# Kernel optimization log

Hardware: AMD Instinct MI355X
Metric: run time of the kernel (lower is better)

Reference implementation:

```python
import jax, jax.numpy as jnp
import numpy as np

N = 500000      # total nodes
C = 256         # in_channels
H = 8           # num_heads
D = 32          # out_channels per head
G = 4096        # number of graphs in the batch


def setup_inputs() -> dict:
    key = jax.random.key(0)
    k1, k2, k3, k4, k5 = jax.random.split(key, 5)
    x = jax.random.normal(k1, (N, C), dtype=jnp.float32)
    batch = jnp.sort(jax.random.randint(k2, (N,), 0, G)).astype(jnp.int64)
    Wg = jax.random.normal(k3, (H, C), dtype=jnp.float32) / np.sqrt(C)
    Wn = jax.random.normal(k4, (H, C, D), dtype=jnp.float32) / np.sqrt(C)
    bn = jax.random.normal(k5, (H, D), dtype=jnp.float32) * 0.01
    return {"x": x, "batch": batch, "Wg": Wg, "Wn": Wn, "bn": bn}


def reference(x, batch, Wg, Wn, bn):
    batch = batch.astype(jnp.int32)
    # Gate logits for all heads at once: [N, H]
    gate = x @ Wg.T
    # Segment-wise (per-graph) stable softmax over nodes, per head
    m = jax.ops.segment_max(gate, batch, num_segments=G)        # [G, H]
    e = jnp.exp(gate - m[batch])                                # [N, H]
    s = jax.ops.segment_sum(e, batch, num_segments=G)           # [G, H]
    alpha = e / s[batch]                                        # [N, H]
    # Per-head value projection: [N, H, D]
    v = jnp.einsum('nc,hcd->nhd', x, Wn) + bn
    # Attention-weighted segment sum -> [G, H, D], concat heads -> [G, H*D]
    out = jax.ops.segment_sum(alpha[:, :, None] * v, batch, num_segments=G)
    return out.reshape(G, H * D)
```

## Files before the change

kernel.cpp:

```cpp
#include <hip/hip_runtime.h>
#include <hip/hip_bf16.h>
#include <cmath>

#define NN 500000
#define CC 256
#define HH 8
#define DD 32
#define GG 4096
#define CH 32

#define OFF_START 0
#define OFF_FLAG  16400

__device__ __forceinline__ int get_batch(const void* b, int i, int is64) {
    return is64 ? (int)((const long long*)b)[i] : ((const int*)b)[i];
}

__global__ void detect_kernel(const int* __restrict__ b32, int n, int* __restrict__ flag) {
    if (threadIdx.x == 0 && blockIdx.x == 0) {
        int a = b32[(n / 2) | 1];
        int b = b32[(n - 2) | 1];
        int c = b32[((n / 2) + (n / 4)) | 1];
        *flag = (a == 0 && b == 0 && c == 0) ? 1 : 0;
    }
}

__global__ void seg_offsets_kernel(const void* __restrict__ batch, const int* __restrict__ flag,
                                   int n, int g_total, int* __restrict__ start) {
    int is64 = *flag;
    int i = blockIdx.x * blockDim.x + threadIdx.x;
    if (i >= n) return;
    int b = get_batch(batch, i, is64);
    int prev = (i == 0) ? -1 : get_batch(batch, i - 1, is64);
    for (int g = prev + 1; g <= b; ++g) start[g] = i;
    if (i == n - 1) {
        for (int g = b + 1; g <= g_total; ++g) start[g] = n;
    }
}

__global__ __launch_bounds__(256) void fused_kernel(const float* __restrict__ x,
                                                    const int* __restrict__ start,
                                                    const float* __restrict__ Wg,
                                                    const float* __restrict__ Wn,
                                                    const float* __restrict__ bn,
                                                    float* __restrict__ out) {
    __shared__ float4 xb4[CH * 64];
    __shared__ float wgxw[HH * CC];
    __shared__ float e_lds[CH * HH];
    __shared__ float red[256];
    __shared__ float inv_s[HH];

    int g = blockIdx.x, t = threadIdx.x;
    int s0 = start[g], s1 = start[g + 1], len = s1 - s0;

    if (len == 0) { out[(size_t)g * (HH * DD) + t] = 0.f; return; }

    float4* wg4l = reinterpret_cast<float4*>(wgxw);
    const float4* wg4 = reinterpret_cast<const float4*>(Wg);
    wg4l[t]       = wg4[t];
    wg4l[t + 256] = wg4[t + 256];

    float acc[HH][4];
#pragma unroll
    for (int h = 0; h < HH; ++h)
#pragma unroll
        for (int e = 0; e < 4; ++e) acc[h][e] = 0.f;
    float s_part = 0.f;

    const int sub = t & 7, oct = t >> 3;
    const int q = t >> 6, cg = t & 63;

    const float4* x4 = reinterpret_cast<const float4*>(x);

    __syncthreads();

    for (int base = 0; base < len; base += CH) {
        int cl = (len - base < CH) ? (len - base) : CH;

        if (oct < cl) {
            const float4* xr = x4 + (size_t)(s0 + base + oct) * (CC / 4);
            float4 xv[8];
#pragma unroll
            for (int j = 0; j < 8; ++j) xv[j] = xr[j * 8 + sub];

            float a8[HH];
#pragma unroll
            for (int h = 0; h < HH; ++h) a8[h] = 0.f;
#pragma unroll
            for (int j = 0; j < 8; ++j) {
                xb4[oct * 64 + j * 8 + sub] = xv[j];
#pragma unroll
                for (int h = 0; h < HH; ++h) {
                    float4 w = wg4l[h * 64 + j * 8 + sub];
                    a8[h] += xv[j].x * w.x + xv[j].y * w.y + xv[j].z * w.z + xv[j].w * w.w;
                }
            }
#pragma unroll
            for (int h = 0; h < HH; ++h) {
                a8[h] += __shfl_xor(a8[h], 1);
                a8[h] += __shfl_xor(a8[h], 2);
                a8[h] += __shfl_xor(a8[h], 4);
            }
            float v = a8[0];
#pragma unroll
            for (int h = 1; h < HH; ++h) v = (sub == h) ? a8[h] : v;
            float ev = expf(v);
            e_lds[oct * 8 + sub] = ev;
            s_part += ev;
        }
        __syncthreads();

        const float4* e4 = reinterpret_cast<const float4*>(e_lds);
        for (int i = q; i < cl; i += 4) {
            float4 xv = xb4[i * 64 + cg];
            float4 a0 = e4[i * 2], a1 = e4[i * 2 + 1];
            acc[0][0] += a0.x * xv.x; acc[0][1] += a0.x * xv.y; acc[0][2] += a0.x * xv.z; acc[0][3] += a0.x * xv.w;
            acc[1][0] += a0.y * xv.x; acc[1][1] += a0.y * xv.y; acc[1][2] += a0.y * xv.z; acc[1][3] += a0.y * xv.w;
            acc[2][0] += a0.z * xv.x; acc[2][1] += a0.z * xv.y; acc[2][2] += a0.z * xv.z; acc[2][3] += a0.z * xv.w;
            acc[3][0] += a0.w * xv.x; acc[3][1] += a0.w * xv.y; acc[3][2] += a0.w * xv.z; acc[3][3] += a0.w * xv.w;
            acc[4][0] += a1.x * xv.x; acc[4][1] += a1.x * xv.y; acc[4][2] += a1.x * xv.z; acc[4][3] += a1.x * xv.w;
            acc[5][0] += a1.y * xv.x; acc[5][1] += a1.y * xv.y; acc[5][2] += a1.y * xv.z; acc[5][3] += a1.y * xv.w;
            acc[6][0] += a1.z * xv.x; acc[6][1] += a1.z * xv.y; acc[6][2] += a1.z * xv.z; acc[6][3] += a1.z * xv.w;
            acc[7][0] += a1.w * xv.x; acc[7][1] += a1.w * xv.y; acc[7][2] += a1.w * xv.z; acc[7][3] += a1.w * xv.w;
        }
        __syncthreads();
    }

    {
#pragma unroll
        for (int off = 8; off < 64; off <<= 1) s_part += __shfl_xor(s_part, off);
        if ((t & 63) < 8) red[(t >> 6) * 8 + sub] = s_part;
    }
#pragma unroll
    for (int h = 0; h < HH; ++h)
        xb4[q * 512 + h * 64 + cg] = make_float4(acc[h][0], acc[h][1], acc[h][2], acc[h][3]);
    __syncthreads();
    if (t < HH) inv_s[t] = 1.f / (red[t] + red[8 + t] + red[16 + t] + red[24 + t]);

    const float* xwf = reinterpret_cast<const float*>(xb4);
    for (int idx = t; idx < HH * CC; idx += 256)
        wgxw[idx] = xwf[idx] + xwf[2048 + idx] + xwf[4096 + idx] + xwf[6144 + idx];
    __syncthreads();

    int ph = t >> 5, pd = t & 31;
    const float* wnp = Wn + (size_t)ph * CC * DD + pd;
    float o = 0.f;
#pragma unroll 8
    for (int c0 = 0; c0 < CC; ++c0) {
        int ce = (c0 + 4 * ph) & 255;
        o += wgxw[ph * 256 + ce] * wnp[(size_t)ce * DD];
    }
    o = bn[ph * DD + pd] + inv_s[ph] * o;
    out[(size_t)g * (HH * DD) + t] = o;
}

extern "C" void kernel_launch(void* const* d_in, const int* in_sizes, int n_in,
                              void* d_out, int out_size, void* d_ws, size_t ws_size,
                              hipStream_t stream) {
    const float* x     = (const float*)d_in[0];
    const void*  batch = d_in[1];
    const float* Wg    = (const float*)d_in[2];
    const float* Wn    = (const float*)d_in[3];
    const float* bn    = (const float*)d_in[4];
    float* out = (float*)d_out;

    char* w = (char*)d_ws;
    int* startp = (int*)(w + OFF_START);
    int* flag   = (int*)(w + OFF_FLAG);

    detect_kernel<<<1, 64, 0, stream>>>((const int*)batch, NN, flag);
    seg_offsets_kernel<<<(NN + 255) / 256, 256, 0, stream>>>(batch, flag, NN, GG, startp);
    fused_kernel<<<GG, 256, 0, stream>>>(x, startp, Wg, Wn, bn, out);
}
```

Baseline: 188.4 us.

## Prefetch next node chunk into registers, stage x and exp weights as bf16

Processes 64 nodes per iteration, with each thread handling two rows. The next chunk's x rows are loaded into registers before the weighted-accumulate phase, so global loads overlap compute. The staged x and exp weights are packed to bf16 in shared memory with an XOR swizzle, which lowers LDS footprint and bank conflicts, and expf is replaced by __expf. In exchange, precision in the accumulation drops to bf16 inputs and register pressure rises from the doubled x buffers.

```diff
diff --git a/kernel.cpp b/kernel.cpp
--- a/kernel.cpp
+++ b/kernel.cpp
@@ -7,7 +7,7 @@
 #define HH 8
 #define DD 32
 #define GG 4096
-#define CH 32
+#define CH2 64
 
 #define OFF_START 0
 #define OFF_FLAG  16400
@@ -38,15 +38,24 @@
     }
 }
 
+__device__ __forceinline__ unsigned pack_bf2(float a, float b) {
+    __hip_bfloat162 h2 = __float22bfloat162_rn(make_float2(a, b));
+    unsigned u;
+    __builtin_memcpy(&u, &h2, 4);
+    return u;
+}
+__device__ __forceinline__ float ubf_lo(unsigned u) { return __uint_as_float(u << 16); }
+__device__ __forceinline__ float ubf_hi(unsigned u) { return __uint_as_float(u & 0xffff0000u); }
+
 __global__ __launch_bounds__(256) void fused_kernel(const float* __restrict__ x,
                                                     const int* __restrict__ start,
                                                     const float* __restrict__ Wg,
                                                     const float* __restrict__ Wn,
                                                     const float* __restrict__ bn,
                                                     float* __restrict__ out) {
-    __shared__ float4 xb4[CH * 64];
+    __shared__ uint2 xb[CH2 * 64];
     __shared__ float wgxw[HH * CC];
-    __shared__ float e_lds[CH * HH];
+    __shared__ uint4 e_bf[CH2];
     __shared__ float red[256];
     __shared__ float inv_s[HH];
 
@@ -60,6 +69,12 @@
     wg4l[t]       = wg4[t];
     wg4l[t + 256] = wg4[t + 256];
 
+    const int sub = t & 7, oct = t >> 3;
+    const int q = t >> 6, cg = t & 63;
+    const int swz = (oct & 1) << 3;
+
+    const float4* x4 = reinterpret_cast<const float4*>(x);
+
     float acc[HH][4];
 #pragma unroll
     for (int h = 0; h < HH; ++h)
@@ -67,77 +82,125 @@
         for (int e = 0; e < 4; ++e) acc[h][e] = 0.f;
     float s_part = 0.f;
 
-    const int sub = t & 7, oct = t >> 3;
-    const int q = t >> 6, cg = t & 63;
-
-    const float4* x4 = reinterpret_cast<const float4*>(x);
-
+    float4 xvA[8], xvB[8];
+    if (oct < len) {
+        const float4* xr = x4 + (size_t)(s0 + oct) * (CC / 4);
+#pragma unroll
+        for (int j = 0; j < 8; ++j) xvA[j] = xr[j * 8 + sub];
+    }
+    if (32 + oct < len) {
+        const float4* xr = x4 + (size_t)(s0 + 32 + oct) * (CC / 4);
+#pragma unroll
+        for (int j = 0; j < 8; ++j) xvB[j] = xr[j * 8 + sub];
+    }
     __syncthreads();
 
-    for (int base = 0; base < len; base += CH) {
-        int cl = (len - base < CH) ? (len - base) : CH;
-
-        if (oct < cl) {
-            const float4* xr = x4 + (size_t)(s0 + base + oct) * (CC / 4);
-            float4 xv[8];
-#pragma unroll
-            for (int j = 0; j < 8; ++j) xv[j] = xr[j * 8 + sub];
-
-            float a8[HH];
-#pragma unroll
-            for (int h = 0; h < HH; ++h) a8[h] = 0.f;
+    for (int base = 0; base < len; base += CH2) {
+        int cl = (len - base < CH2) ? (len - base) : CH2;
+        bool vA = oct < cl, vB = (32 + oct) < cl;
+
+        float a8A[HH], a8B[HH];
+#pragma unroll
+        for (int h = 0; h < HH; ++h) { a8A[h] = 0.f; a8B[h] = 0.f; }
+#pragma unroll
+        for (int j = 0; j < 8; ++j) {
+#pragma unroll
+            for (int h = 0; h < HH; ++h) {
+                float4 w = wg4l[h * 64 + j * 8 + sub];
+                a8A[h] += xvA[j].x * w.x + xvA[j].y * w.y + xvA[j].z * w.z + xvA[j].w * w.w;
+                a8B[h] += xvB[j].x * w.x + xvB[j].y * w.y + xvB[j].z * w.z + xvB[j].w * w.w;
+            }
+        }
+#pragma unroll
+        for (int h = 0; h < HH; ++h) {
+            a8A[h] += __shfl_xor(a8A[h], 1);
+            a8A[h] += __shfl_xor(a8A[h], 2);
+            a8A[h] += __shfl_xor(a8A[h], 4);
+            a8B[h] += __shfl_xor(a8B[h], 1);
+            a8B[h] += __shfl_xor(a8B[h], 2);
+            a8B[h] += __shfl_xor(a8B[h], 4);
+        }
+
+        int h0 = (sub & 3) * 2;
+        float eA0 = __expf(a8A[h0]), eA1 = __expf(a8A[h0 + 1]);
+        float eB0 = __expf(a8B[h0]), eB1 = __expf(a8B[h0 + 1]);
+        if (vA) s_part += (sub < 4) ? eA0 : eA1;
+        if (vB) s_part += (sub < 4) ? eB0 : eB1;
+        unsigned* eW = reinterpret_cast<unsigned*>(e_bf);
+        if (sub < 4) {
+            if (vA) eW[oct * 4 + sub]        = pack_bf2(eA0, eA1);
+            if (vB) eW[(32 + oct) * 4 + sub] = pack_bf2(eB0, eB1);
+        }
+
+        if (vA) {
 #pragma unroll
             for (int j = 0; j < 8; ++j) {
-                xb4[oct * 64 + j * 8 + sub] = xv[j];
-#pragma unroll
-                for (int h = 0; h < HH; ++h) {
-                    float4 w = wg4l[h * 64 + j * 8 + sub];
-                    a8[h] += xv[j].x * w.x + xv[j].y * w.y + xv[j].z * w.z + xv[j].w * w.w;
-                }
+                uint2 p;
+                p.x = pack_bf2(xvA[j].x, xvA[j].y);
+                p.y = pack_bf2(xvA[j].z, xvA[j].w);
+                xb[oct * 64 + ((j * 8 + sub) ^ swz)] = p;
             }
-#pragma unroll
-            for (int h = 0; h < HH; ++h) {
-                a8[h] += __shfl_xor(a8[h], 1);
-                a8[h] += __shfl_xor(a8[h], 2);
-                a8[h] += __shfl_xor(a8[h], 4);
+        }
+        if (vB) {
+#pragma unroll
+            for (int j = 0; j < 8; ++j) {
+                uint2 p;
+                p.x = pack_bf2(xvB[j].x, xvB[j].y);
+                p.y = pack_bf2(xvB[j].z, xvB[j].w);
+                xb[(32 + oct) * 64 + ((j * 8 + sub) ^ swz)] = p;
             }
-            float v = a8[0];
-#pragma unroll
-            for (int h = 1; h < HH; ++h) v = (sub == h) ? a8[h] : v;
-            float ev = expf(v);
-            e_lds[oct * 8 + sub] = ev;
-            s_part += ev;
+        }
+
+        int nb = base + CH2;
+        if (nb + oct < len) {
+            const float4* xr = x4 + (size_t)(s0 + nb + oct) * (CC / 4);
+#pragma unroll
+            for (int j = 0; j < 8; ++j) xvA[j] = xr[j * 8 + sub];
+        }
+        if (nb + 32 + oct < len) {
+            const float4* xr = x4 + (size_t)(s0 + nb + 32 + oct) * (CC / 4);
+#pragma unroll
+            for (int j = 0; j < 8; ++j) xvB[j] = xr[j * 8 + sub];
         }
         __syncthreads();
 
-        const float4* e4 = reinterpret_cast<const float4*>(e_lds);
+#pragma unroll 4
         for (int i = q; i < cl; i += 4) {
-            float4 xv = xb4[i * 64 + cg];
-            float4 a0 = e4[i * 2], a1 = e4[i * 2 + 1];
-            acc[0][0] += a0.x * xv.x; acc[0][1] += a0.x * xv.y; acc[0][2] += a0.x * xv.z; acc[0][3] += a0.x * xv.w;
-            acc[1][0] += a0.y * xv.x; acc[1][1] += a0.y * xv.y; acc[1][2] += a0.y * xv.z; acc[1][3] += a0.y * xv.w;
-            acc[2][0] += a0.z * xv.x; acc[2][1] += a0.z * xv.y; acc[2][2] += a0.z * xv.z; acc[2][3] += a0.z * xv.w;
-            acc[3][0] += a0.w * xv.x; acc[3][1] += a0.w * xv.y; acc[3][2] += a0.w * xv.z; acc[3][3] += a0.w * xv.w;
-            acc[4][0] += a1.x * xv.x; acc[4][1] += a1.x * xv.y; acc[4][2] += a1.x * xv.z; acc[4][3] += a1.x * xv.w;
-            acc[5][0] += a1.y * xv.x; acc[5][1] += a1.y * xv.y; acc[5][2] += a1.y * xv.z; acc[5][3] += a1.y * xv.w;
-            acc[6][0] += a1.z * xv.x; acc[6][1] += a1.z * xv.y; acc[6][2] += a1.z * xv.z; acc[6][3] += a1.z * xv.w;
-            acc[7][0] += a1.w * xv.x; acc[7][1] += a1.w * xv.y; acc[7][2] += a1.w * xv.z; acc[7][3] += a1.w * xv.w;
+            uint4 eu = e_bf[i];
+            uint2 xu = xb[i * 64 + (cg ^ ((i & 1) << 3))];
+            float x0 = ubf_lo(xu.x), x1 = ubf_hi(xu.x);
+            float x2 = ubf_lo(xu.y), x3 = ubf_hi(xu.y);
+            float e0 = ubf_lo(eu.x), e1 = ubf_hi(eu.x);
+            float e2 = ubf_lo(eu.y), e3 = ubf_hi(eu.y);
+            float e4 = ubf_lo(eu.z), e5 = ubf_hi(eu.z);
+            float e6 = ubf_lo(eu.w), e7 = ubf_hi(eu.w);
+            acc[0][0] += e0 * x0; acc[0][1] += e0 * x1; acc[0][2] += e0 * x2; acc[0][3] += e0 * x3;
+            acc[1][0] += e1 * x0; acc[1][1] += e1 * x1; acc[1][2] += e1 * x2; acc[1][3] += e1 * x3;
+            acc[2][0] += e2 * x0; acc[2][1] += e2 * x1; acc[2][2] += e2 * x2; acc[2][3] += e2 * x3;
+            acc[3][0] += e3 * x0; acc[3][1] += e3 * x1; acc[3][2] += e3 * x2; acc[3][3] += e3 * x3;
+            acc[4][0] += e4 * x0; acc[4][1] += e4 * x1; acc[4][2] += e4 * x2; acc[4][3] += e4 * x3;
+            acc[5][0] += e5 * x0; acc[5][1] += e5 * x1; acc[5][2] += e5 * x2; acc[5][3] += e5 * x3;
+            acc[6][0] += e6 * x0; acc[6][1] += e6 * x1; acc[6][2] += e6 * x2; acc[6][3] += e6 * x3;
+            acc[7][0] += e7 * x0; acc[7][1] += e7 * x1; acc[7][2] += e7 * x2; acc[7][3] += e7 * x3;
         }
         __syncthreads();
     }
 
-    {
-#pragma unroll
-        for (int off = 8; off < 64; off <<= 1) s_part += __shfl_xor(s_part, off);
-        if ((t & 63) < 8) red[(t >> 6) * 8 + sub] = s_part;
-    }
+#pragma unroll
+    for (int off = 8; off < 64; off <<= 1) s_part += __shfl_xor(s_part, off);
+    if ((t & 63) < 8) red[(t >> 6) * 8 + sub] = s_part;
+
+    float4* xw4 = reinterpret_cast<float4*>(xb);
 #pragma unroll
     for (int h = 0; h < HH; ++h)
-        xb4[q * 512 + h * 64 + cg] = make_float4(acc[h][0], acc[h][1], acc[h][2], acc[h][3]);
+        xw4[q * 512 + h * 64 + cg] = make_float4(acc[h][0], acc[h][1], acc[h][2], acc[h][3]);
     __syncthreads();
-    if (t < HH) inv_s[t] = 1.f / (red[t] + red[8 + t] + red[16 + t] + red[24 + t]);
-
-    const float* xwf = reinterpret_cast<const float*>(xb4);
+    if (t < HH) {
+        int myh = (t < 4) ? 2 * t : 2 * (t - 4) + 1;
+        inv_s[myh] = 1.f / (red[t] + red[8 + t] + red[16 + t] + red[24 + t]);
+    }
+
+    const float* xwf = reinterpret_cast<const float*>(xb);
     for (int idx = t; idx < HH * CC; idx += 256)
         wgxw[idx] = xwf[idx] + xwf[2048 + idx] + xwf[4096 + idx] + xwf[6144 + idx];
     __syncthreads();
```

Result: slower. 367.5 us (+95.1%).

## Compute gate logits with bf16 MFMA using per-wave independent node tiles

Applied to the files above, without the earlier changes.

The gate projection moves from scalar FP32 dot products with shuffle reductions to `mfma_f32_16x16x32_bf16`, with Wg held in registers as bf16 fragments. Each wave now handles its own 16-node tile in a private, swizzled bf16 LDS slice, which removes the block-wide barriers from the main loop. The exp weights and the staged x are also stored as bf16, and launch bounds request higher occupancy. The aim is to cut ALU and LDS work and synchronisation so the kernel nears the x-read bandwidth limit, at the cost of bf16 rounding in both the logits and the weighted sums.

```diff
diff --git a/kernel.cpp b/kernel.cpp
--- a/kernel.cpp
+++ b/kernel.cpp
@@ -7,7 +7,9 @@
 #define HH 8
 #define DD 32
 #define GG 4096
-#define CH 32
+
+typedef short bf16x8 __attribute__((ext_vector_type(8)));
+typedef float f32x4 __attribute__((ext_vector_type(4)));
 
 #define OFF_START 0
 #define OFF_FLAG  16400
@@ -38,16 +40,24 @@
     }
 }
 
-__global__ __launch_bounds__(256) void fused_kernel(const float* __restrict__ x,
-                                                    const int* __restrict__ start,
-                                                    const float* __restrict__ Wg,
-                                                    const float* __restrict__ Wn,
-                                                    const float* __restrict__ bn,
-                                                    float* __restrict__ out) {
-    __shared__ float4 xb4[CH * 64];
-    __shared__ float wgxw[HH * CC];
-    __shared__ float e_lds[CH * HH];
-    __shared__ float red[256];
+__device__ __forceinline__ unsigned pack_bf2(float a, float b) {
+    __hip_bfloat162 h2 = __float22bfloat162_rn(make_float2(a, b));
+    unsigned u;
+    __builtin_memcpy(&u, &h2, 4);
+    return u;
+}
+__device__ __forceinline__ float ubf_lo(unsigned u) { return __uint_as_float(u << 16); }
+__device__ __forceinline__ float ubf_hi(unsigned u) { return __uint_as_float(u & 0xffff0000u); }
+
+__global__ __launch_bounds__(256, 4) void fused_kernel(const float* __restrict__ x,
+                                                       const int* __restrict__ start,
+                                                       const float* __restrict__ Wg,
+                                                       const float* __restrict__ Wn,
+                                                       const float* __restrict__ bn,
+                                                       float* __restrict__ out) {
+    __shared__ float4 xb4[2048];
+    __shared__ uint4 e_q[64];
+    __shared__ float red[32];
     __shared__ float inv_s[HH];
 
     int g = blockIdx.x, t = threadIdx.x;
@@ -55,10 +65,31 @@
 
     if (len == 0) { out[(size_t)g * (HH * DD) + t] = 0.f; return; }
 
-    float4* wg4l = reinterpret_cast<float4*>(wgxw);
-    const float4* wg4 = reinterpret_cast<const float4*>(Wg);
-    wg4l[t]       = wg4[t];
-    wg4l[t + 256] = wg4[t + 256];
+    const int w  = t >> 6;
+    const int l  = t & 63;
+    const int lr = l & 15;
+    const int lk = l >> 4;
+
+    bf16x8 wb[8];
+    {
+        int hc = lr & 7;
+        const float4* wp4 = reinterpret_cast<const float4*>(Wg + hc * CC + lk * 8);
+#pragma unroll
+        for (int tt = 0; tt < 8; ++tt) {
+            float4 wa = wp4[tt * 8], wbv = wp4[tt * 8 + 1];
+            unsigned u01 = pack_bf2(wa.x, wa.y), u23 = pack_bf2(wa.z, wa.w);
+            unsigned u45 = pack_bf2(wbv.x, wbv.y), u67 = pack_bf2(wbv.z, wbv.w);
+            if (lr < 8) {
+                wb[tt][0] = (short)(u01 & 0xffff); wb[tt][1] = (short)(u01 >> 16);
+                wb[tt][2] = (short)(u23 & 0xffff); wb[tt][3] = (short)(u23 >> 16);
+                wb[tt][4] = (short)(u45 & 0xffff); wb[tt][5] = (short)(u45 >> 16);
+                wb[tt][6] = (short)(u67 & 0xffff); wb[tt][7] = (short)(u67 >> 16);
+            } else {
+#pragma unroll
+                for (int j = 0; j < 8; ++j) wb[tt][j] = 0;
+            }
+        }
+    }
 
     float acc[HH][4];
 #pragma unroll
@@ -67,79 +98,93 @@
         for (int e = 0; e < 4; ++e) acc[h][e] = 0.f;
     float s_part = 0.f;
 
-    const int sub = t & 7, oct = t >> 3;
-    const int q = t >> 6, cg = t & 63;
-
+    char* slice = (char*)xb4 + w * 8192;
     const float4* x4 = reinterpret_cast<const float4*>(x);
-
+    const int sn = l >> 3, sub = l & 7;
+
+    for (int tb = w * 16; tb < len; tb += 64) {
+        int tl = (len - tb < 16) ? (len - tb) : 16;
+
+#pragma unroll
+        for (int pass = 0; pass < 2; ++pass) {
+            int n = pass * 8 + sn;
+            if (n < tl) {
+                const float4* xr = x4 + (size_t)(s0 + tb + n) * (CC / 4) + sub;
+                float4 v[8];
+#pragma unroll
+                for (int j = 0; j < 8; ++j) v[j] = xr[j * 8];
+                char* rb = slice + n * 512;
+                unsigned swz = (unsigned)((n & 7) << 4);
+#pragma unroll
+                for (int j = 0; j < 8; ++j) {
+                    uint2 p;
+                    p.x = pack_bf2(v[j].x, v[j].y);
+                    p.y = pack_bf2(v[j].z, v[j].w);
+                    *reinterpret_cast<uint2*>(rb + (((unsigned)((j * 8 + sub) * 8)) ^ swz)) = p;
+                }
+            }
+        }
+
+        f32x4 d = {0.f, 0.f, 0.f, 0.f};
+        {
+            char* rb = slice + lr * 512;
+            unsigned swz = (unsigned)((lr & 7) << 4);
+#pragma unroll
+            for (int tt = 0; tt < 8; ++tt) {
+                bf16x8 a = *reinterpret_cast<bf16x8*>(rb + (((unsigned)(lk * 16 + tt * 64)) ^ swz));
+                d = __builtin_amdgcn_mfma_f32_16x16x32_bf16(a, wb[tt], d, 0, 0, 0);
+            }
+        }
+
+        {
+            unsigned short* ep = reinterpret_cast<unsigned short*>(e_q) + (w * 16) * 8;
+#pragma unroll
+            for (int r = 0; r < 4; ++r) {
+                int n = lk * 4 + r;
+                float e = 0.f;
+                if (n < tl && lr < 8) { e = __expf(d[r]); s_part += e; }
+                if (lr < 8) ep[n * 8 + lr] = (unsigned short)(pack_bf2(e, 0.f) & 0xffff);
+            }
+        }
+
+        {
+            const uint4* eq = e_q + w * 16;
+            for (int i = 0; i < tl; ++i) {
+                uint4 eu = eq[i];
+                unsigned swz = (unsigned)((i & 7) << 4);
+                uint2 xu = *reinterpret_cast<uint2*>(slice + i * 512 + (((unsigned)(l * 8)) ^ swz));
+                float x0 = ubf_lo(xu.x), x1 = ubf_hi(xu.x);
+                float x2 = ubf_lo(xu.y), x3 = ubf_hi(xu.y);
+                float e0 = ubf_lo(eu.x), e1 = ubf_hi(eu.x);
+                float e2 = ubf_lo(eu.y), e3 = ubf_hi(eu.y);
+                float e4 = ubf_lo(eu.z), e5 = ubf_hi(eu.z);
+                float e6 = ubf_lo(eu.w), e7 = ubf_hi(eu.w);
+                acc[0][0] += e0 * x0; acc[0][1] += e0 * x1; acc[0][2] += e0 * x2; acc[0][3] += e0 * x3;
+                acc[1][0] += e1 * x0; acc[1][1] += e1 * x1; acc[1][2] += e1 * x2; acc[1][3] += e1 * x3;
+                acc[2][0] += e2 * x0; acc[2][1] += e2 * x1; acc[2][2] += e2 * x2; acc[2][3] += e2 * x3;
+                acc[3][0] += e3 * x0; acc[3][1] += e3 * x1; acc[3][2] += e3 * x2; acc[3][3] += e3 * x3;
+                acc[4][0] += e4 * x0; acc[4][1] += e4 * x1; acc[4][2] += e4 * x2; acc[4][3] += e4 * x3;
+                acc[5][0] += e5 * x0; acc[5][1] += e5 * x1; acc[5][2] += e5 * x2; acc[5][3] += e5 * x3;
+                acc[6][0] += e6 * x0; acc[6][1] += e6 * x1; acc[6][2] += e6 * x2; acc[6][3] += e6 * x3;
+                acc[7][0] += e7 * x0; acc[7][1] += e7 * x1; acc[7][2] += e7 * x2; acc[7][3] += e7 * x3;
+            }
+        }
+    }
+
+    s_part += __shfl_xor(s_part, 16);
+    s_part += __shfl_xor(s_part, 32);
+    if (l < 8) red[w * 8 + l] = s_part;
+
+#pragma unroll
+    for (int h = 0; h < HH; ++h)
+        xb4[w * 512 + h * 64 + l] = make_float4(acc[h][0], acc[h][1], acc[h][2], acc[h][3]);
     __syncthreads();
 
-    for (int base = 0; base < len; base += CH) {
-        int cl = (len - base < CH) ? (len - base) : CH;
-
-        if (oct < cl) {
-            const float4* xr = x4 + (size_t)(s0 + base + oct) * (CC / 4);
-            float4 xv[8];
-#pragma unroll
-            for (int j = 0; j < 8; ++j) xv[j] = xr[j * 8 + sub];
-
-            float a8[HH];
-#pragma unroll
-            for (int h = 0; h < HH; ++h) a8[h] = 0.f;
-#pragma unroll
-            for (int j = 0; j < 8; ++j) {
-                xb4[oct * 64 + j * 8 + sub] = xv[j];
-#pragma unroll
-                for (int h = 0; h < HH; ++h) {
-                    float4 w = wg4l[h * 64 + j * 8 + sub];
-                    a8[h] += xv[j].x * w.x + xv[j].y * w.y + xv[j].z * w.z + xv[j].w * w.w;
-                }
-            }
-#pragma unroll
-            for (int h = 0; h < HH; ++h) {
-                a8[h] += __shfl_xor(a8[h], 1);
-                a8[h] += __shfl_xor(a8[h], 2);
-                a8[h] += __shfl_xor(a8[h], 4);
-            }
-            float v = a8[0];
-#pragma unroll
-            for (int h = 1; h < HH; ++h) v = (sub == h) ? a8[h] : v;
-            float ev = expf(v);
-            e_lds[oct * 8 + sub] = ev;
-            s_part += ev;
-        }
-        __syncthreads();
-
-        const float4* e4 = reinterpret_cast<const float4*>(e_lds);
-        for (int i = q; i < cl; i += 4) {
-            float4 xv = xb4[i * 64 + cg];
-            float4 a0 = e4[i * 2], a1 = e4[i * 2 + 1];
-            acc[0][0] += a0.x * xv.x; acc[0][1] += a0.x * xv.y; acc[0][2] += a0.x * xv.z; acc[0][3] += a0.x * xv.w;
-            acc[1][0] += a0.y * xv.x; acc[1][1] += a0.y * xv.y; acc[1][2] += a0.y * xv.z; acc[1][3] += a0.y * xv.w;
-            acc[2][0] += a0.z * xv.x; acc[2][1] += a0.z * xv.y; acc[2][2] += a0.z * xv.z; acc[2][3] += a0.z * xv.w;
-            acc[3][0] += a0.w * xv.x; acc[3][1] += a0.w * xv.y; acc[3][2] += a0.w * xv.z; acc[3][3] += a0.w * xv.w;
-            acc[4][0] += a1.x * xv.x; acc[4][1] += a1.x * xv.y; acc[4][2] += a1.x * xv.z; acc[4][3] += a1.x * xv.w;
-            acc[5][0] += a1.y * xv.x; acc[5][1] += a1.y * xv.y; acc[5][2] += a1.y * xv.z; acc[5][3] += a1.y * xv.w;
-            acc[6][0] += a1.z * xv.x; acc[6][1] += a1.z * xv.y; acc[6][2] += a1.z * xv.z; acc[6][3] += a1.z * xv.w;
-            acc[7][0] += a1.w * xv.x; acc[7][1] += a1.w * xv.y; acc[7][2] += a1.w * xv.z; acc[7][3] += a1.w * xv.w;
-        }
-        __syncthreads();
-    }
-
-    {
-#pragma unroll
-        for (int off = 8; off < 64; off <<= 1) s_part += __shfl_xor(s_part, off);
-        if ((t & 63) < 8) red[(t >> 6) * 8 + sub] = s_part;
-    }
-#pragma unroll
-    for (int h = 0; h < HH; ++h)
-        xb4[q * 512 + h * 64 + cg] = make_float4(acc[h][0], acc[h][1], acc[h][2], acc[h][3]);
-    __syncthreads();
     if (t < HH) inv_s[t] = 1.f / (red[t] + red[8 + t] + red[16 + t] + red[24 + t]);
 
-    const float* xwf = reinterpret_cast<const float*>(xb4);
+    float* xwf = reinterpret_cast<float*>(xb4);
     for (int idx = t; idx < HH * CC; idx += 256)
-        wgxw[idx] = xwf[idx] + xwf[2048 + idx] + xwf[4096 + idx] + xwf[6144 + idx];
+        xwf[idx] = xwf[idx] + xwf[2048 + idx] + xwf[4096 + idx] + xwf[6144 + idx];
     __syncthreads();
 
     int ph = t >> 5, pd = t & 31;
@@ -148,7 +193,7 @@
 #pragma unroll 8
     for (int c0 = 0; c0 < CC; ++c0) {
         int ce = (c0 + 4 * ph) & 255;
-        o += wgxw[ph * 256 + ce] * wnp[(size_t)ce * DD];
+        o += xwf[ph * 256 + ce] * wnp[(size_t)ce * DD];
     }
     o = bn[ph * DD + pd] + inv_s[ph] * o;
     out[(size_t)g * (HH * DD) + t] = o;
```

Result: slower. 224.1 us (+19.0%).
